# Kernel tuning notes

Hardware: AMD Instinct MI355X
Metric: run time of the kernel (lower is better)

The kernel has to match this reference:

```python
import jax, jax.numpy as jnp
import numpy as np

BQ, BK = 128, 64  # SpargeAttn-style Q/K block sizes
NEG = -1e30


def _block_mask(q, k, simthreshd1, cdfthreshd, scale):
    """Mean-similarity block selection: a (q-block, k-block) pair is pruned only
    when both blocks are self-similar (mean cosine sim to block mean exceeds the
    per-head simthreshd1) AND it is not in the top-CDF mass (cdfthreshd) of the
    compressed block-level softmax."""
    B, H, L, D = q.shape
    nq, nk = L // BQ, L // BK
    qb = q.reshape(B, H, nq, BQ, D)
    kb = k.reshape(B, H, nk, BK, D)
    qm = qb.mean(3)  # [B,H,nq,D] block means
    km = kb.mean(3)  # [B,H,nk,D]

    def blocksim(xb, xm):
        xn = xb / (jnp.linalg.norm(xb, axis=-1, keepdims=True) + 1e-6)
        mn = xm / (jnp.linalg.norm(xm, axis=-1, keepdims=True) + 1e-6)
        return jnp.einsum('bhntd,bhnd->bhnt', xn, mn).mean(-1)  # [B,H,n]

    th = simthreshd1[None, :, None]
    comp_q = blocksim(qb, qm) > th  # [B,H,nq] self-similar q blocks
    comp_k = blocksim(kb, km) > th  # [B,H,nk]

    # compressed attention over block means, then CDF-based top-mass selection
    p = jax.nn.softmax(jnp.einsum('bhqd,bhkd->bhqk', qm, km) * scale, axis=-1)
    order = jnp.argsort(-p, axis=-1)
    sp = jnp.take_along_axis(p, order, axis=-1)
    csum = jnp.cumsum(sp, axis=-1)
    keep_sorted = (csum - sp) < cdfthreshd[None, :, None, None]  # prefix covering tau
    rank = jnp.argsort(order, axis=-1)  # inverse permutation
    selected = jnp.take_along_axis(keep_sorted, rank, axis=-1)  # [B,H,nq,nk]

    return selected | ~(comp_q[..., :, None] & comp_k[..., None, :])


def setup_inputs() -> dict:
    key = jax.random.key(0)
    kq, kk, kv, kc = jax.random.split(key, 4)
    B, H, L, D = 1, 16, 2048, 64
    return {
        'q': jax.random.normal(kq, (B, H, L, D), dtype=jnp.float32),
        'k': jax.random.normal(kk, (B, H, L, D), dtype=jnp.float32),
        'v': jax.random.normal(kv, (B, H, L, D), dtype=jnp.float32),
        'simthreshd1': jnp.zeros((H,), dtype=jnp.float32),
        'cdfthreshd': jax.random.uniform(kc, (H,), dtype=jnp.float32),
    }


def reference(q, k, v, simthreshd1, cdfthreshd):
    B, H, L, D = q.shape
    scale = 1.0 / np.sqrt(D).astype(np.float32)
    # smooth_k: subtract per-(B,H) key mean (softmax-invariant shift, matches kernel)
    k = k - k.mean(axis=-2, keepdims=True)
    bmask = _block_mask(q, k, simthreshd1, cdfthreshd, scale)  # [B,H,nq,nk] bool
    mask_tok = jnp.repeat(jnp.repeat(bmask, BQ, axis=2), BK, axis=3)  # [B,H,L,L]
    s = jnp.einsum('bhqd,bhkd->bhqk', q, k) * scale
    s = jnp.where(mask_tok, s, NEG)
    p = jax.nn.softmax(s, axis=-1)
    return jnp.einsum('bhqk,bhkd->bhqd', p, v)
```

## Files before the change

kernel.cpp:

```cpp
#include <hip/hip_runtime.h>

#define HH 16
#define LL 2048
#define DD 64
#define BQ 128
#define BK 64
#define NQ (LL/BQ)
#define NK (LL/BK)
#define SCALE 0.125f
#define QSCALE (0.125f * 1.44269504f)

typedef __attribute__((ext_vector_type(8))) short s8v;
typedef __attribute__((ext_vector_type(4))) float f4v;

static __device__ __forceinline__ ushort f2bf(float x) {
    unsigned u = __float_as_uint(x);
    u += 0x7fff + ((u >> 16) & 1);
    return (ushort)(u >> 16);
}

__global__ void kmean1_kernel(const float* __restrict__ k, float* __restrict__ kpart) {
    int b = blockIdx.x;
    int h = blockIdx.y;
    int t = threadIdx.x;
    int d = t & 63, c = t >> 6;
    const float* kh = k + ((size_t)h*LL + (size_t)b*256) * DD;
    float s = 0.f;
    for (int l = c*64; l < c*64 + 64; ++l) s += kh[(size_t)l * DD + d];
    __shared__ float red[4][64];
    red[c][d] = s;
    __syncthreads();
    if (t < 64) kpart[((size_t)h*8 + b)*64 + t] = red[0][t]+red[1][t]+red[2][t]+red[3][t];
}

__global__ __launch_bounds__(128) void stats_kernel(
        const float* __restrict__ q, const float* __restrict__ k, const float* __restrict__ v,
        const float* __restrict__ kpart, const float* __restrict__ simth,
        float* __restrict__ qm, float* __restrict__ km,
        int* __restrict__ compq, int* __restrict__ compk,
        ushort* __restrict__ qb, ushort* __restrict__ kb, ushort* __restrict__ vTb) {
    __shared__ __align__(16) char smem[34304];
    int h = blockIdx.y, t = threadIdx.x;

    if ((int)blockIdx.x < NQ) {
        int qi = blockIdx.x;
        float (*xs)[DD+1] = (float(*)[DD+1])smem;
        float* mean = (float*)(smem + 33280);
        float* red  = (float*)(smem + 33536);
        size_t row = (size_t)h*LL + (size_t)qi*BQ + t;
        const float* rp = q + row * DD;
        float x[DD]; float n2 = 0.f;
        #pragma unroll
        for (int d = 0; d < DD; d += 4) {
            float4 v4 = *(const float4*)(rp + d);
            x[d]=v4.x; x[d+1]=v4.y; x[d+2]=v4.z; x[d+3]=v4.w;
            n2 += v4.x*v4.x + v4.y*v4.y + v4.z*v4.z + v4.w*v4.w;
        }
        #pragma unroll
        for (int d = 0; d < DD; d += 4) {
            ushort4 o;
            o.x = f2bf(x[d]*QSCALE);   o.y = f2bf(x[d+1]*QSCALE);
            o.z = f2bf(x[d+2]*QSCALE); o.w = f2bf(x[d+3]*QSCALE);
            *(ushort4*)(qb + row*DD + d) = o;
        }
        #pragma unroll
        for (int d = 0; d < DD; ++d) xs[t][d] = x[d];
        __syncthreads();
        {
            int d = t & 63, hf = t >> 6;
            float s = 0.f;
            for (int r = hf*64; r < hf*64 + 64; ++r) s += xs[r][d];
            red[t] = s;
        }
        __syncthreads();
        if (t < DD) mean[t] = (red[t] + red[64 + t]) * (1.0f/BQ);
        __syncthreads();
        float dot = 0.f, m2 = 0.f;
        #pragma unroll
        for (int d = 0; d < DD; ++d) { dot += x[d]*mean[d]; m2 += mean[d]*mean[d]; }
        float cs = dot / ((sqrtf(n2) + 1e-6f) * (sqrtf(m2) + 1e-6f));
        __syncthreads();
        red[t] = cs; __syncthreads();
        for (int sft = BQ/2; sft > 0; sft >>= 1) {
            if (t < sft) red[t] += red[t + sft];
            __syncthreads();
        }
        if (t == 0) compq[h*NQ + qi] = (red[0] * (1.0f/BQ)) > simth[h] ? 1 : 0;
        if (t < DD) qm[((size_t)h*NQ + qi)*DD + t] = mean[t];
    } else {
        int ki = blockIdx.x - NQ;
        float* mu_s = (float*)smem;
        float (*xs)[DD+1] = (float(*)[DD+1])(smem + 256);
        ushort (*vs)[66]  = (ushort(*)[66])(smem + 256 + 16640);
        float* mean = (float*)(smem + 256 + 16640 + 8448);
        float* red  = (float*)(smem + 256 + 16640 + 8448 + 256);
        if (t < 64) {
            float s = 0.f;
            #pragma unroll
            for (int b = 0; b < 8; ++b) s += kpart[((size_t)h*8 + b)*64 + t];
            mu_s[t] = s * (1.0f/LL);
        }
        __syncthreads();
        size_t rowb = (size_t)h*LL + (size_t)ki*BK;
        float x[DD]; float n2 = 0.f;
        if (t < 64) {
            const float* rp = k + (rowb + t) * DD;
            #pragma unroll
            for (int d = 0; d < DD; d += 4) {
                float4 v4 = *(const float4*)(rp + d);
                v4.x -= mu_s[d]; v4.y -= mu_s[d+1]; v4.z -= mu_s[d+2]; v4.w -= mu_s[d+3];
                x[d]=v4.x; x[d+1]=v4.y; x[d+2]=v4.z; x[d+3]=v4.w;
                n2 += v4.x*v4.x + v4.y*v4.y + v4.z*v4.z + v4.w*v4.w;
            }
            #pragma unroll
            for (int d = 0; d < DD; d += 4) {
                ushort4 o;
                o.x = f2bf(x[d]);   o.y = f2bf(x[d+1]);
                o.z = f2bf(x[d+2]); o.w = f2bf(x[d+3]);
                *(ushort4*)(kb + (rowb + t)*DD + d) = o;
            }
            #pragma unroll
            for (int d = 0; d < DD; ++d) xs[t][d] = x[d];
        } else {
            int tk = t - 64;
            const float* vp = v + (rowb + tk) * DD;
            #pragma unroll
            for (int d = 0; d < DD; d += 4) {
                float4 v4 = *(const float4*)(vp + d);
                vs[tk][d]   = f2bf(v4.x); vs[tk][d+1] = f2bf(v4.y);
                vs[tk][d+2] = f2bf(v4.z); vs[tk][d+3] = f2bf(v4.w);
            }
        }
        __syncthreads();
        if (t < 64) {
            size_t vbase = ((size_t)h*DD + t)*LL + (size_t)ki*64;
            #pragma unroll
            for (int r8 = 0; r8 < 64; r8 += 8) {
                s8v o;
                #pragma unroll
                for (int e = 0; e < 8; ++e) o[e] = (short)vs[r8+e][t];
                *(s8v*)(vTb + vbase + r8) = o;
            }
            float s = 0.f;
            for (int r = 0; r < BK; ++r) s += xs[r][t];
            mean[t] = s * (1.0f/BK);
        }
        __syncthreads();
        if (t < 64) {
            float dot = 0.f, m2 = 0.f;
            #pragma unroll
            for (int d = 0; d < DD; ++d) { dot += x[d]*mean[d]; m2 += mean[d]*mean[d]; }
            float cs = dot / ((sqrtf(n2) + 1e-6f) * (sqrtf(m2) + 1e-6f));
            red[t] = cs;
        }
        __syncthreads();
        for (int sft = 32; sft > 0; sft >>= 1) {
            if (t < sft) red[t] += red[t + sft];
            __syncthreads();
        }
        if (t == 0) compk[h*NK + ki] = (red[0] * (1.0f/BK)) > simth[h] ? 1 : 0;
        if (t < 64) km[((size_t)h*NK + ki)*DD + t] = mean[t];
    }
}

__global__ __launch_bounds__(256, 2) void attn_kernel(
        const ushort* __restrict__ qb, const ushort* __restrict__ kb,
        const ushort* __restrict__ vTb,
        const float* __restrict__ qm, const float* __restrict__ km,
        const int* __restrict__ compq, const int* __restrict__ compk,
        const float* __restrict__ cdfth, float* __restrict__ out) {
    __shared__ __align__(16) char shmem[69632];
    ushort* pl = (ushort*)shmem + (threadIdx.x >> 6) * 64 * 72;
    float*  Ob = (float*)shmem;
    float*  mb = (float*)(shmem + 67584);
    float*  lb = (float*)(shmem + 68608);

    int bid  = blockIdx.x;
    int slot = bid >> 3;
    int h    = ((slot >> 5) << 3) | (bid & 7);
    int qi   = (slot & 31) >> 1;
    int half = slot & 1;
    int tid  = threadIdx.x;
    int w    = tid >> 6;
    int l    = tid & 63;
    int lo = l & 15, hi = l >> 4;
    int r0 = qi*BQ + half*64;

    const ushort* qh = qb  + (size_t)h*LL*DD;
    const ushort* kh = kb  + (size_t)h*LL*DD;
    const ushort* vh = vTb + (size_t)h*DD*LL;

    s8v qf[4][2];
    #pragma unroll
    for (int qt = 0; qt < 4; ++qt)
        #pragma unroll
        for (int kk = 0; kk < 2; ++kk)
            qf[qt][kk] = *(const s8v*)(qh + (size_t)(r0 + qt*16 + lo)*DD + kk*32 + hi*8);

    unsigned msk;
    {
        float* ebw = (float*)pl;
        float* pbw = ebw + 32;
        int j = l & 31;
        const float* qv = qm + ((size_t)h*NQ + qi)*DD;
        const float* kv = km + ((size_t)h*NK + j)*DD;
        float s = 0.f;
        #pragma unroll
        for (int d = 0; d < DD; d += 4) {
            float4 a = *(const float4*)(qv + d);
            float4 b = *(const float4*)(kv + d);
            s += a.x*b.x; s += a.y*b.y; s += a.z*b.z; s += a.w*b.w;
        }
        s *= SCALE;
        float mx = s;
        #pragma unroll
        for (int xm = 1; xm <= 16; xm <<= 1) mx = fmaxf(mx, __shfl_xor(mx, xm, 32));
        float e = expf(s - mx);
        ebw[j] = e;
        float den = 0.f;
        #pragma unroll
        for (int i = 0; i < 32; ++i) den += ebw[i];
        float p = e / den;
        pbw[j] = p;
        float mass = 0.f;
        #pragma unroll
        for (int i = 0; i < 32; ++i) {
            float pi = pbw[i];
            if (pi > p || (pi == p && i < j)) mass += pi;
        }
        int keep = (mass < cdfth[h]) || !(compq[h*NQ+qi] && compk[h*NK+j]);
        unsigned long long bal = __ballot(keep != 0);
        msk = (unsigned)bal;
    }

    f4v O[4][4];
    float m[4], lsum[4];
    #pragma unroll
    for (int qt = 0; qt < 4; ++qt) {
        m[qt] = -1e30f; lsum[qt] = 0.f;
        #pragma unroll
        for (int dt = 0; dt < 4; ++dt) O[qt][dt] = (f4v){0.f,0.f,0.f,0.f};
    }

    unsigned mm = msk; int rank = 0;
    while (mm) {
        int j = __ffs(mm) - 1; mm &= mm - 1;
        if (((rank++) & 3) != w) continue;

        const ushort* kbj = kh + (size_t)j*BK*DD;
        const ushort* vbj = vh + (size_t)j*BK;

        s8v kf[4][2];
        #pragma unroll
        for (int kt = 0; kt < 4; ++kt)
            #pragma unroll
            for (int kk = 0; kk < 2; ++kk)
                kf[kt][kk] = *(const s8v*)(kbj + (size_t)(kt*16 + lo)*DD + kk*32 + hi*8);

        f4v S[4][4];
        #pragma unroll
        for (int kt = 0; kt < 4; ++kt)
            #pragma unroll
            for (int qt = 0; qt < 4; ++qt)
                S[kt][qt] = (f4v){0.f,0.f,0.f,0.f};
        __builtin_amdgcn_s_setprio(1);
        #pragma unroll
        for (int kk = 0; kk < 2; ++kk)
            #pragma unroll
            for (int kt = 0; kt < 4; ++kt)
                #pragma unroll
                for (int qt = 0; qt < 4; ++qt)
                    S[kt][qt] = __builtin_amdgcn_mfma_f32_16x16x32_bf16(kf[kt][kk], qf[qt][kk], S[kt][qt], 0, 0, 0);
        __builtin_amdgcn_s_setprio(0);

        s8v vf[2][4];
        #pragma unroll
        for (int kk = 0; kk < 2; ++kk)
            #pragma unroll
            for (int dt = 0; dt < 4; ++dt)
                vf[kk][dt] = *(const s8v*)(vbj + (size_t)(dt*16 + lo)*LL + kk*32 + hi*8);

        float pm[4];
        #pragma unroll
        for (int qt = 0; qt < 4; ++qt) {
            float a0 = fmaxf(fmaxf(S[0][qt][0],S[0][qt][1]), fmaxf(S[0][qt][2],S[0][qt][3]));
            float a1 = fmaxf(fmaxf(S[1][qt][0],S[1][qt][1]), fmaxf(S[1][qt][2],S[1][qt][3]));
            float a2 = fmaxf(fmaxf(S[2][qt][0],S[2][qt][1]), fmaxf(S[2][qt][2],S[2][qt][3]));
            float a3 = fmaxf(fmaxf(S[3][qt][0],S[3][qt][1]), fmaxf(S[3][qt][2],S[3][qt][3]));
            float p = fmaxf(fmaxf(a0,a1), fmaxf(a2,a3));
            p = fmaxf(p, __shfl_xor(p, 16));
            p = fmaxf(p, __shfl_xor(p, 32));
            pm[qt] = p;
        }
        bool grow = (pm[0] > m[0]+8.0f) | (pm[1] > m[1]+8.0f) |
                    (pm[2] > m[2]+8.0f) | (pm[3] > m[3]+8.0f);
        if (__any(grow)) {
            float alpha[4];
            #pragma unroll
            for (int qt = 0; qt < 4; ++qt) {
                float mn = fmaxf(m[qt], pm[qt]);
                alpha[qt] = __builtin_amdgcn_exp2f(m[qt] - mn);
                lsum[qt] *= alpha[qt];
                m[qt] = mn;
            }
            #pragma unroll
            for (int qt = 0; qt < 4; ++qt)
                #pragma unroll
                for (int r = 0; r < 4; ++r) {
                    float a = __shfl(alpha[qt], hi*4 + r);
                    #pragma unroll
                    for (int dt = 0; dt < 4; ++dt) O[qt][dt][r] *= a;
                }
        }
        #pragma unroll
        for (int qt = 0; qt < 4; ++qt) {
            float ps = 0.f;
            #pragma unroll
            for (int kt = 0; kt < 4; ++kt) {
                float p0 = __builtin_amdgcn_exp2f(S[kt][qt][0] - m[qt]);
                float p1 = __builtin_amdgcn_exp2f(S[kt][qt][1] - m[qt]);
                float p2 = __builtin_amdgcn_exp2f(S[kt][qt][2] - m[qt]);
                float p3 = __builtin_amdgcn_exp2f(S[kt][qt][3] - m[qt]);
                ps += (p0 + p1) + (p2 + p3);
                unsigned c01, c23;
                asm("v_cvt_pk_bf16_f32 %0, %1, %2" : "=v"(c01) : "v"(p0), "v"(p1));
                asm("v_cvt_pk_bf16_f32 %0, %1, %2" : "=v"(c23) : "v"(p2), "v"(p3));
                *(uint2*)&pl[(qt*16 + lo)*72 + kt*16 + hi*4] = make_uint2(c01, c23);
            }
            lsum[qt] += ps;
        }
        __builtin_amdgcn_s_setprio(1);
        #pragma unroll
        for (int qt = 0; qt < 4; ++qt)
            #pragma unroll
            for (int kk = 0; kk < 2; ++kk) {
                s8v pa = *(const s8v*)&pl[(qt*16 + lo)*72 + kk*32 + hi*8];
                #pragma unroll
                for (int dt = 0; dt < 4; ++dt)
                    O[qt][dt] = __builtin_amdgcn_mfma_f32_16x16x32_bf16(pa, vf[kk][dt], O[qt][dt], 0, 0, 0);
            }
        __builtin_amdgcn_s_setprio(0);
    }

    #pragma unroll
    for (int qt = 0; qt < 4; ++qt) {
        lsum[qt] += __shfl_xor(lsum[qt], 16);
        lsum[qt] += __shfl_xor(lsum[qt], 32);
    }

    __syncthreads();

    if (hi == 0) {
        #pragma unroll
        for (int qt = 0; qt < 4; ++qt) {
            mb[w*64 + qt*16 + lo] = m[qt];
            lb[w*64 + qt*16 + lo] = lsum[qt];
        }
    }
    #pragma unroll
    for (int qt = 0; qt < 4; ++qt)
        #pragma unroll
        for (int dt = 0; dt < 4; ++dt)
            #pragma unroll
            for (int r = 0; r < 4; ++r)
                Ob[w*4224 + (qt*16 + hi*4 + r)*66 + dt*16 + lo] = O[qt][dt][r];
    __syncthreads();

    {
        int q = l;
        float mw0 = mb[q], mw1 = mb[64+q], mw2 = mb[128+q], mw3 = mb[192+q];
        float ms = fmaxf(fmaxf(mw0,mw1), fmaxf(mw2,mw3));
        float c0 = __builtin_amdgcn_exp2f(mw0 - ms);
        float c1 = __builtin_amdgcn_exp2f(mw1 - ms);
        float c2 = __builtin_amdgcn_exp2f(mw2 - ms);
        float c3 = __builtin_amdgcn_exp2f(mw3 - ms);
        float ls = lb[q]*c0 + lb[64+q]*c1 + lb[128+q]*c2 + lb[192+q]*c3;
        float inv = 1.0f / ls;
        float* orow = out + ((size_t)h*LL + r0 + q)*DD + w*16;
        #pragma unroll
        for (int i4 = 0; i4 < 4; ++i4) {
            float4 o;
            #pragma unroll
            for (int e = 0; e < 4; ++e) {
                int d = w*16 + i4*4 + e;
                float acc = Ob[q*66 + d]*c0 + Ob[4224 + q*66 + d]*c1
                          + Ob[8448 + q*66 + d]*c2 + Ob[12672 + q*66 + d]*c3;
                ((float*)&o)[e] = acc * inv;
            }
            *(float4*)(orow + i4*4) = o;
        }
    }
}

extern "C" void kernel_launch(void* const* d_in, const int* in_sizes, int n_in,
                              void* d_out, int out_size, void* d_ws, size_t ws_size,
                              hipStream_t stream) {
    const float* q     = (const float*)d_in[0];
    const float* k     = (const float*)d_in[1];
    const float* v     = (const float*)d_in[2];
    const float* simth = (const float*)d_in[3];
    const float* cdfth = (const float*)d_in[4];
    float* out = (float*)d_out;

    float* ws    = (float*)d_ws;
    float* kpart = ws;
    float* qm    = kpart + HH*8*64;
    float* km    = qm + HH*NQ*DD;
    int*   compq = (int*)(km + HH*NK*DD);
    int*   compk = compq + HH*NQ;
    size_t off = (size_t)((char*)(compk + HH*NK) - (char*)d_ws);
    off = (off + 15) & ~(size_t)15;
    ushort* qbuf = (ushort*)((char*)d_ws + off);
    ushort* kbuf = qbuf + (size_t)HH*LL*DD;
    ushort* vTb  = kbuf + (size_t)HH*LL*DD;

    kmean1_kernel<<<dim3(8, HH), 256, 0, stream>>>(k, kpart);
    stats_kernel<<<dim3(NQ + NK, HH), 128, 0, stream>>>(q, k, v, kpart, simth,
                                                        qm, km, compq, compk,
                                                        qbuf, kbuf, vTb);
    attn_kernel<<<dim3(NQ*2*HH), 256, 0, stream>>>(qbuf, kbuf, vTb,
                                                   qm, km, compq, compk, cdfth, out);
}
```

Before: 72.13 us.

## Split KV blocks across eight waves per block with two-stage bf16 merge

```diff
diff --git a/kernel.cpp b/kernel.cpp
--- a/kernel.cpp
+++ b/kernel.cpp
@@ -17,6 +17,9 @@
     unsigned u = __float_as_uint(x);
     u += 0x7fff + ((u >> 16) & 1);
     return (ushort)(u >> 16);
+}
+static __device__ __forceinline__ float bf2f(ushort u) {
+    return __uint_as_float(((unsigned)u) << 16);
 }
 
 __global__ void kmean1_kernel(const float* __restrict__ k, float* __restrict__ kpart) {
@@ -163,17 +166,17 @@
     }
 }
 
-__global__ __launch_bounds__(256, 2) void attn_kernel(
+__global__ __launch_bounds__(512, 2) void attn_kernel(
         const ushort* __restrict__ qb, const ushort* __restrict__ kb,
         const ushort* __restrict__ vTb,
         const float* __restrict__ qm, const float* __restrict__ km,
         const int* __restrict__ compq, const int* __restrict__ compk,
         const float* __restrict__ cdfth, float* __restrict__ out) {
-    __shared__ __align__(16) char shmem[69632];
-    ushort* pl = (ushort*)shmem + (threadIdx.x >> 6) * 64 * 72;
+    __shared__ __align__(16) char shmem[75776];
+    ushort* pl = (ushort*)shmem + (threadIdx.x >> 6) * 4608;
     float*  Ob = (float*)shmem;
-    float*  mb = (float*)(shmem + 67584);
-    float*  lb = (float*)(shmem + 68608);
+    float*  mb = (float*)(shmem + 73728);
+    float*  lb = (float*)(shmem + 74752);
 
     int bid  = blockIdx.x;
     int slot = bid >> 3;
@@ -245,7 +248,7 @@
     unsigned mm = msk; int rank = 0;
     while (mm) {
         int j = __ffs(mm) - 1; mm &= mm - 1;
-        if (((rank++) & 3) != w) continue;
+        if (((rank++) & 7) != w) continue;
 
         const ushort* kbj = kh + (size_t)j*BK*DD;
         const ushort* vbj = vh + (size_t)j*BK;
@@ -349,24 +352,72 @@
     }
 
     __syncthreads();
-
-    if (hi == 0) {
+    if (w >= 4) {
+        ushort* myO = pl;
+        float* myM = (float*)(pl + 4096);
+        float* myL = (float*)(pl + 4224);
+        #pragma unroll
+        for (int qt = 0; qt < 4; ++qt)
+            #pragma unroll
+            for (int dt = 0; dt < 4; ++dt)
+                #pragma unroll
+                for (int r = 0; r < 4; ++r)
+                    myO[(qt*16 + hi*4 + r)*64 + dt*16 + lo] = f2bf(O[qt][dt][r]);
+        if (hi == 0) {
+            #pragma unroll
+            for (int qt = 0; qt < 4; ++qt) {
+                myM[qt*16 + lo] = m[qt];
+                myL[qt*16 + lo] = lsum[qt];
+            }
+        }
+    }
+    __syncthreads();
+    if (w < 4) {
+        const ushort* pO = (const ushort*)shmem + (w + 4) * 4608;
+        const float* pM = (const float*)(pO + 4096);
+        const float* pL = (const float*)(pO + 4224);
+        float aq[4], bq[4];
         #pragma unroll
         for (int qt = 0; qt < 4; ++qt) {
-            mb[w*64 + qt*16 + lo] = m[qt];
-            lb[w*64 + qt*16 + lo] = lsum[qt];
-        }
-    }
-    #pragma unroll
-    for (int qt = 0; qt < 4; ++qt)
-        #pragma unroll
-        for (int dt = 0; dt < 4; ++dt)
-            #pragma unroll
-            for (int r = 0; r < 4; ++r)
-                Ob[w*4224 + (qt*16 + hi*4 + r)*66 + dt*16 + lo] = O[qt][dt][r];
+            float mp = pM[qt*16 + lo], lp = pL[qt*16 + lo];
+            float mn = fmaxf(m[qt], mp);
+            float a = __builtin_amdgcn_exp2f(m[qt] - mn);
+            float b = __builtin_amdgcn_exp2f(mp - mn);
+            lsum[qt] = lsum[qt]*a + lp*b;
+            m[qt] = mn; aq[qt] = a; bq[qt] = b;
+        }
+        #pragma unroll
+        for (int qt = 0; qt < 4; ++qt)
+            #pragma unroll
+            for (int r = 0; r < 4; ++r) {
+                float ar = __shfl(aq[qt], hi*4 + r);
+                float br = __shfl(bq[qt], hi*4 + r);
+                #pragma unroll
+                for (int dt = 0; dt < 4; ++dt) {
+                    float op = bf2f(pO[(qt*16 + hi*4 + r)*64 + dt*16 + lo]);
+                    O[qt][dt][r] = O[qt][dt][r]*ar + op*br;
+                }
+            }
+    }
     __syncthreads();
-
-    {
+    if (w < 4) {
+        if (hi == 0) {
+            #pragma unroll
+            for (int qt = 0; qt < 4; ++qt) {
+                mb[w*64 + qt*16 + lo] = m[qt];
+                lb[w*64 + qt*16 + lo] = lsum[qt];
+            }
+        }
+        #pragma unroll
+        for (int qt = 0; qt < 4; ++qt)
+            #pragma unroll
+            for (int dt = 0; dt < 4; ++dt)
+                #pragma unroll
+                for (int r = 0; r < 4; ++r)
+                    Ob[w*4224 + (qt*16 + hi*4 + r)*66 + dt*16 + lo] = O[qt][dt][r];
+    }
+    __syncthreads();
+    if (tid < 256) {
         int q = l;
         float mw0 = mb[q], mw1 = mb[64+q], mw2 = mb[128+q], mw3 = mb[192+q];
         float ms = fmaxf(fmaxf(mw0,mw1), fmaxf(mw2,mw3));
@@ -418,6 +469,6 @@
     stats_kernel<<<dim3(NQ + NK, HH), 128, 0, stream>>>(q, k, v, kpart, simth,
                                                         qm, km, compq, compk,
                                                         qbuf, kbuf, vTb);
-    attn_kernel<<<dim3(NQ*2*HH), 256, 0, stream>>>(qbuf, kbuf, vTb,
+    attn_kernel<<<dim3(NQ*2*HH), 512, 0, stream>>>(qbuf, kbuf, vTb,
                                                    qm, km, compq, compk, cdfth, out);
 }
```

Result: slower. 83.76 us (+16.1%).
